# Kernel optimization log

Measured on AMD Instinct MI355X. Metric: run time of the kernel, lower is better.

## Reference

```python
import jax, jax.numpy as jnp
import numpy as np

B, T, X, H, Z, P = 256, 512, 64, 256, 64, 32

_PARAM_SHAPES = [
    ("phi_x_W1", (X, P)), ("phi_x_b1", (P,)), ("phi_x_W2", (P, P)), ("phi_x_b2", (P,)),
    ("phi_z_W", (Z, Z)), ("phi_z_b", (Z,)),
    ("enc_W1", (P + H, H)), ("enc_b1", (H,)), ("enc_W2", (H, H)), ("enc_b2", (H,)),
    ("enc_mean_W", (H, Z)), ("enc_mean_b", (Z,)), ("enc_std_W", (H, Z)), ("enc_std_b", (Z,)),
    ("prior_W", (H, H)), ("prior_b", (H,)),
    ("prior_mean_W", (H, Z)), ("prior_mean_b", (Z,)), ("prior_std_W", (H, Z)), ("prior_std_b", (Z,)),
    ("dec_W1", (Z + H, H)), ("dec_b1", (H,)), ("dec_W2", (H, H)), ("dec_b2", (H,)),
    ("dec_mean_W", (H, X)), ("dec_mean_b", (X,)), ("dec_std_W", (H, X)), ("dec_std_b", (X,)),
    ("gru_K", (P + Z, 3 * H)), ("gru_R", (H, 3 * H)), ("gru_b", (2, 3 * H)),
]


def setup_inputs() -> dict:
    key = jax.random.key(0)
    ks = jax.random.split(key, 4 + len(_PARAM_SHAPES))
    d = {
        "x": jax.random.normal(ks[0], (B, T, X), jnp.float32),
        "y": jax.random.normal(ks[1], (B, T, Z), jnp.float32),
        "domain_labels": jax.random.uniform(ks[2], (B, T, Z), dtype=jnp.float32),
        "eps": jax.random.normal(ks[3], (B, T, Z), jnp.float32),
    }
    for i, (name, shp) in enumerate(_PARAM_SHAPES):
        d[name] = jax.random.normal(ks[4 + i], shp, jnp.float32) * 0.05
    return d


def _vrnn_forward(x, eps,
                  phi_x_W1, phi_x_b1, phi_x_W2, phi_x_b2,
                  phi_z_W, phi_z_b,
                  enc_W1, enc_b1, enc_W2, enc_b2,
                  enc_mean_W, enc_mean_b, enc_std_W, enc_std_b,
                  prior_W, prior_b, prior_mean_W, prior_mean_b, prior_std_W, prior_std_b,
                  dec_W1, dec_b1, dec_W2, dec_b2,
                  dec_mean_W, dec_mean_b, dec_std_W, dec_std_b,
                  gru_K, gru_R, gru_b):
    relu, sp, sig = jax.nn.relu, jax.nn.softplus, jax.nn.sigmoid

    def dense(a, W, b):
        return a @ W + b

    def step(h, inp):
        x_t, eps_t = inp  # [B, X], [B, Z]
        phi_x_t = relu(dense(relu(dense(x_t, phi_x_W1, phi_x_b1)), phi_x_W2, phi_x_b2))
        enc_h = relu(dense(relu(dense(jnp.concatenate([phi_x_t, h], 1), enc_W1, enc_b1)), enc_W2, enc_b2))
        enc_mean_t = dense(enc_h, enc_mean_W, enc_mean_b)
        enc_std_t = sp(dense(enc_h, enc_std_W, enc_std_b))
        pri_h = relu(dense(h, prior_W, prior_b))
        pri_mean_t = dense(pri_h, prior_mean_W, prior_mean_b)
        pri_std_t = sp(dense(pri_h, prior_std_W, prior_std_b))
        z_t = eps_t * enc_std_t + enc_mean_t  # reparameterized sample
        phi_z_t = relu(dense(z_t, phi_z_W, phi_z_b))
        dec_h = relu(dense(relu(dense(jnp.concatenate([phi_z_t, h], 1), dec_W1, dec_b1)), dec_W2, dec_b2))
        dec_mean_t = dense(dec_h, dec_mean_W, dec_mean_b)
        dec_std_t = sp(dense(dec_h, dec_std_W, dec_std_b))
        # Keras GRU cell (reset_after=True): separate input/recurrent biases
        mx = jnp.concatenate([phi_x_t, phi_z_t], 1) @ gru_K + gru_b[0]
        mh = h @ gru_R + gru_b[1]
        xz, xr, xh = jnp.split(mx, 3, axis=1)
        hz, hr, hh = jnp.split(mh, 3, axis=1)
        zg = sig(xz + hz)
        rg = sig(xr + hr)
        h_cand = jnp.tanh(xh + rg * hh)
        h_new = zg * h + (1.0 - zg) * h_cand
        return h_new, (z_t, phi_x_t, enc_mean_t, enc_std_t, dec_mean_t, dec_std_t, pri_mean_t, pri_std_t)

    h0 = jnp.zeros((x.shape[0], gru_R.shape[0]), x.dtype)
    xs = (jnp.swapaxes(x, 0, 1), jnp.swapaxes(eps, 0, 1))  # time-major for scan
    _, outs = jax.lax.scan(step, h0, xs)
    return tuple(jnp.swapaxes(o, 0, 1) for o in outs)  # back to [B, T, .]


def reference(x, y, domain_labels, eps,
              phi_x_W1, phi_x_b1, phi_x_W2, phi_x_b2,
              phi_z_W, phi_z_b,
              enc_W1, enc_b1, enc_W2, enc_b2,
              enc_mean_W, enc_mean_b, enc_std_W, enc_std_b,
              prior_W, prior_b, prior_mean_W, prior_mean_b, prior_std_W, prior_std_b,
              dec_W1, dec_b1, dec_W2, dec_b2,
              dec_mean_W, dec_mean_b, dec_std_W, dec_std_b,
              gru_K, gru_R, gru_b):
    # y and domain_labels are accepted (as in the original __call__) but do not
    # affect the forward math.
    (y_pred, phi_x, enc_mean, enc_std, dec_mean, dec_std, pri_mean, pri_std) = _vrnn_forward(
        x, eps,
        phi_x_W1, phi_x_b1, phi_x_W2, phi_x_b2,
        phi_z_W, phi_z_b,
        enc_W1, enc_b1, enc_W2, enc_b2,
        enc_mean_W, enc_mean_b, enc_std_W, enc_std_b,
        prior_W, prior_b, prior_mean_W, prior_mean_b, prior_std_W, prior_std_b,
        dec_W1, dec_b1, dec_W2, dec_b2,
        dec_mean_W, dec_mean_b, dec_std_W, dec_std_b,
        gru_K, gru_R, gru_b)
    return (y_pred, phi_x, (enc_mean, enc_std), (dec_mean, dec_std), (pri_mean, pri_std))
```

## Files before the change

kernel.cpp:

```cpp
#include <hip/hip_runtime.h>


typedef _Float16 f16;
typedef _Float16 f16x2 __attribute__((ext_vector_type(2)));
typedef _Float16 f16x8 __attribute__((ext_vector_type(8)));
typedef float    f32x4 __attribute__((ext_vector_type(4)));

#define B_  256
#define T_  512
#define BT_ 131072

#define OYP   0u
#define OPHIX 8388608u
#define OENCM 12582912u
#define OENCS 20971520u
#define ODECM 29360128u
#define ODECS 37748736u
#define OPRIM 46137344u
#define OPRIS 54525952u

#define WS_PHIX16 0ull
#define WS_H16    8388608ull
#define WS_PZ16   75497472ull
#define WS_WHB    92274688ull
#define WS_W1TOP  92798976ull
#define WS_KTOP   92815360ull
#define WS_KBOT   92864512ull
#define WS_ENCW2  92962816ull
#define WS_HEADS  93093888ull
#define WS_PHIZW  93159424ull
#define WS_DECW1T 93167616ull
#define WS_DECW2T 93331456ull
#define WS_DECHT  93462528ull
#define WS_PRIWT  93528064ull
#define WS_PRIHT  93659136ull

#if defined(__has_builtin)
#if __has_builtin(__builtin_amdgcn_fdot2)
#define HAVE_FDOT2 1
#endif
#endif

__device__ __forceinline__ float dot8(uint4 w, uint4 h, float acc) {
#ifdef HAVE_FDOT2
    union { uint4 u; f16x2 p[4]; } a, b;
    a.u = w; b.u = h;
    acc = __builtin_amdgcn_fdot2(a.p[0], b.p[0], acc, false);
    acc = __builtin_amdgcn_fdot2(a.p[1], b.p[1], acc, false);
    acc = __builtin_amdgcn_fdot2(a.p[2], b.p[2], acc, false);
    acc = __builtin_amdgcn_fdot2(a.p[3], b.p[3], acc, false);
#else
    union { uint4 u; f16 h8[8]; } a, b;
    a.u = w; b.u = h;
#pragma unroll
    for (int i = 0; i < 8; ++i) acc += (float)a.h8[i] * (float)b.h8[i];
#endif
    return acc;
}

__device__ __forceinline__ float softplus_f(float v) {
    return (v > 15.f) ? v : log1pf(expf(v));
}
__device__ __forceinline__ float sigmoid_f(float v) {
    return 1.f / (1.f + expf(-v));
}

__global__ void pack_loop(const float* __restrict__ src, f16* __restrict__ dst,
                          int K, int Nsrc, int Ndst, int coloff) {
    int idx = blockIdx.x * 256 + threadIdx.x;
    if (idx >= K * Nsrc) return;
    int k = idx / Nsrc, j = idx - k * Nsrc;
    dst[((size_t)(k >> 3) * Ndst + coloff + j) * 8 + (k & 7)] = (f16)src[idx];
}

__global__ void pack_T(const float* __restrict__ src, f16* __restrict__ dst,
                       int K, int N, int noff, int Kd) {
    int idx = blockIdx.x * 256 + threadIdx.x;
    if (idx >= K * N) return;
    int k = idx / N, n = idx - k * N;
    dst[(size_t)(noff + n) * Kd + k] = (f16)src[idx];
}

__global__ void phi_x_kernel(const float* __restrict__ x,
                             const float* __restrict__ W1, const float* __restrict__ b1,
                             const float* __restrict__ W2, const float* __restrict__ b2,
                             float* __restrict__ dout, f16* __restrict__ phix16) {
    size_t row = (size_t)blockIdx.x * 256 + threadIdx.x;
    const float* xr = x + row * 64;
    float l1[32];
#pragma unroll
    for (int j = 0; j < 32; ++j) l1[j] = b1[j];
#pragma unroll 4
    for (int k = 0; k < 64; ++k) {
        float xv = xr[k];
#pragma unroll
        for (int j = 0; j < 32; ++j) l1[j] += xv * W1[k * 32 + j];
    }
#pragma unroll
    for (int j = 0; j < 32; ++j) l1[j] = fmaxf(l1[j], 0.f);
#pragma unroll 4
    for (int j = 0; j < 32; ++j) {
        float acc = b2[j];
#pragma unroll
        for (int k = 0; k < 32; ++k) acc += l1[k] * W2[k * 32 + j];
        acc = fmaxf(acc, 0.f);
        dout[OPHIX + row * 32 + j] = acc;
        phix16[row * 32 + j] = (f16)acc;
    }
}

__launch_bounds__(512)
__global__ void vrnn_recurrent(
    const f16* __restrict__ whb,
    const f16* __restrict__ w1topb,
    const f16* __restrict__ ktopb,
    const f16* __restrict__ kbotb,
    const f16* __restrict__ encw2b,
    const f16* __restrict__ headsb,
    const f16* __restrict__ phizwb,
    const float* __restrict__ enc_b1, const float* __restrict__ enc_b2,
    const float* __restrict__ enc_mean_b, const float* __restrict__ enc_std_b,
    const float* __restrict__ phi_z_b, const float* __restrict__ gru_b,
    const f16* __restrict__ phix16, const float* __restrict__ eps,
    f16* __restrict__ h16, f16* __restrict__ pz16, float* __restrict__ dout) {

    const int tid = threadIdx.x;
    const int r0 = blockIdx.x * 2;

    __shared__ __align__(16) f16 h_sh[2][256];
    __shared__ __align__(16) f16 e1s[2][256];
    __shared__ __align__(16) f16 ehs[2][256];
    __shared__ __align__(16) f16 zps[2][64];
    __shared__ __align__(16) f16 pzs[2][64];
    __shared__ __align__(16) f16 phixs[2][32];
    __shared__ float hf[2][256];
    __shared__ float hs[2][768];
    __shared__ float xsm[2][768];
    __shared__ float ps[1024];
    __shared__ float sb_e1[256], sb_e2[256], sb_hm[128], sb_pz[64];
    __shared__ float sb_bk[768], sb_br[768];

    if (tid < 256) {
        sb_e1[tid] = enc_b1[tid];
        sb_e2[tid] = enc_b2[tid];
        h_sh[0][tid] = (f16)0.f; h_sh[1][tid] = (f16)0.f;
        hf[0][tid] = 0.f; hf[1][tid] = 0.f;
    }
    if (tid < 128) sb_hm[tid] = (tid < 64) ? enc_mean_b[tid] : enc_std_b[tid - 64];
    if (tid < 64)  sb_pz[tid] = phi_z_b[tid];
    { int i = tid; if (i < 768) { sb_bk[i] = gru_b[i]; sb_br[i] = gru_b[768 + i]; } }
    if (tid >= 256) { int i = tid - 256 + 512; if (i < 768) { sb_bk[i] = gru_b[i]; sb_br[i] = gru_b[768 + i]; } }
    if (tid < 32) {
        int r = tid >> 4, d = tid & 15;
        ((unsigned int*)phixs[r])[d] =
            ((const unsigned int*)(phix16 + (size_t)(r0 + r) * T_ * 32))[d];
    }
    float eps_reg = 0.f;
    if (tid < 128) {
        int r = tid >> 6, c = tid & 63;
        eps_reg = eps[((size_t)(r0 + r) * T_) * 64 + c];
    }
    __syncthreads();

    const int mA = (tid >= 256) ? (tid - 256) : -1;
    const int mB = 256 + tid;

    const uint4* whu   = (const uint4*)whb;
    const uint4* w1tu  = (const uint4*)w1topb;
    const uint4* ktu   = (const uint4*)ktopb;
    const uint4* kbu   = (const uint4*)kbotb;
    const uint4* ew2u  = (const uint4*)encw2b;
    const uint4* hdu   = (const uint4*)headsb;
    const uint4* pzwu  = (const uint4*)phizwb;

    for (int t = 0; t < T_; ++t) {
        float a0, a1, b0, b1;
        if (tid < 256) { a0 = sb_e1[tid]; } else { a0 = sb_br[tid - 256]; }
        a1 = a0;
        b0 = sb_br[mB]; b1 = b0;
        const uint4* h0p = (const uint4*)h_sh[0];
        const uint4* h1p = (const uint4*)h_sh[1];
#pragma unroll 4
        for (int kc = 0; kc < 32; ++kc) {
            uint4 hv0 = h0p[kc], hv1 = h1p[kc];
            uint4 wa = whu[kc * 1024 + tid];
            uint4 wb = whu[kc * 1024 + 512 + tid];
            a0 = dot8(wa, hv0, a0); a1 = dot8(wa, hv1, a1);
            b0 = dot8(wb, hv0, b0); b1 = dot8(wb, hv1, b1);
        }
        float xA0 = 0.f, xA1 = 0.f, xB0, xB1;
        xB0 = sb_bk[mB]; xB1 = xB0;
        if (mA >= 0) { xA0 = sb_bk[mA]; xA1 = xA0; }
        const uint4* px0p = (const uint4*)phixs[0];
        const uint4* px1p = (const uint4*)phixs[1];
#pragma unroll
        for (int kc = 0; kc < 4; ++kc) {
            uint4 p0 = px0p[kc], p1 = px1p[kc];
            uint4 wB = ktu[kc * 768 + mB];
            xB0 = dot8(wB, p0, xB0); xB1 = dot8(wB, p1, xB1);
            if (mA >= 0) {
                uint4 wA = ktu[kc * 768 + mA];
                xA0 = dot8(wA, p0, xA0); xA1 = dot8(wA, p1, xA1);
            }
        }
        if (tid < 256) {
#pragma unroll
            for (int kc = 0; kc < 4; ++kc) {
                uint4 p0 = px0p[kc], p1 = px1p[kc];
                uint4 w = w1tu[kc * 256 + tid];
                a0 = dot8(w, p0, a0); a1 = dot8(w, p1, a1);
            }
            e1s[0][tid] = (f16)fmaxf(a0, 0.f);
            e1s[1][tid] = (f16)fmaxf(a1, 0.f);
        } else {
            hs[0][tid - 256] = a0; hs[1][tid - 256] = a1;
        }
        hs[0][mB] = b0; hs[1][mB] = b1;
        __syncthreads();

        {
            int c = tid & 255, kh = tid >> 8;
            float p0 = 0.f, p1 = 0.f;
            const uint4* e0p = (const uint4*)e1s[0];
            const uint4* e1p = (const uint4*)e1s[1];
#pragma unroll 4
            for (int i = 0; i < 16; ++i) {
                int kc = kh * 16 + i;
                uint4 w = ew2u[kc * 256 + c];
                p0 = dot8(w, e0p[kc], p0);
                p1 = dot8(w, e1p[kc], p1);
            }
            ps[(0 * 2 + kh) * 256 + c] = p0;
            ps[(2 + kh) * 256 + c] = p1;
        }
        __syncthreads();
        {
            int r = tid >> 8, j = tid & 255;
            float v = ps[(r * 2) * 256 + j] + ps[(r * 2 + 1) * 256 + j] + sb_e2[j];
            ehs[r][j] = (f16)fmaxf(v, 0.f);
        }
        __syncthreads();

        {
            int c2 = tid & 127, kq = tid >> 7;
            float p0 = 0.f, p1 = 0.f;
            const uint4* h0e = (const uint4*)ehs[0];
            const uint4* h1e = (const uint4*)ehs[1];
#pragma unroll 4
            for (int i = 0; i < 8; ++i) {
                int kc = kq * 8 + i;
                uint4 w = hdu[kc * 128 + c2];
                p0 = dot8(w, h0e[kc], p0);
                p1 = dot8(w, h1e[kc], p1);
            }
            ps[kq * 128 + c2] = p0;
            ps[(4 + kq) * 128 + c2] = p1;
        }
        __syncthreads();
        if (tid < 128) {
            int r = tid >> 6, c = tid & 63;
            float m = sb_hm[c], s = sb_hm[64 + c];
#pragma unroll
            for (int kq = 0; kq < 4; ++kq) {
                m += ps[(r * 4 + kq) * 128 + c];
                s += ps[(r * 4 + kq) * 128 + 64 + c];
            }
            float sp = softplus_f(s);
            float z = eps_reg * sp + m;
            size_t bt = (size_t)(r0 + r) * T_ + t;
            dout[OENCM + bt * 64 + c] = m;
            dout[OENCS + bt * 64 + c] = sp;
            dout[OYP + bt * 64 + c] = z;
            zps[r][c] = (f16)z;
        }
        __syncthreads();

        {
            int c = tid & 63, k8 = tid >> 6;
            uint4 w = pzwu[k8 * 64 + c];
            ps[k8 * 64 + c]       = dot8(w, ((const uint4*)zps[0])[k8], 0.f);
            ps[(8 + k8) * 64 + c] = dot8(w, ((const uint4*)zps[1])[k8], 0.f);
        }
        __syncthreads();
        if (tid < 128) {
            int r = tid >> 6, c = tid & 63;
            float v = sb_pz[c];
#pragma unroll
            for (int k = 0; k < 8; ++k) v += ps[(r * 8 + k) * 64 + c];
            v = fmaxf(v, 0.f);
            pzs[r][c] = (f16)v;
            size_t bt = (size_t)(r0 + r) * T_ + t;
            pz16[bt * 64 + c] = (f16)v;
            if (t + 1 < T_)
                eps_reg = eps[((size_t)(r0 + r) * T_ + (t + 1)) * 64 + c];
        } else if (tid < 160 && (t + 1 < T_)) {
            int r = (tid - 128) >> 4, d = (tid - 128) & 15;
            ((unsigned int*)phixs[r])[d] =
                ((const unsigned int*)(phix16 + ((size_t)(r0 + r) * T_ + (t + 1)) * 32))[d];
        }
        __syncthreads();

        {
            const uint4* p0p = (const uint4*)pzs[0];
            const uint4* p1p = (const uint4*)pzs[1];
#pragma unroll
            for (int kc = 0; kc < 8; ++kc) {
                uint4 p0 = p0p[kc], p1 = p1p[kc];
                uint4 wB = kbu[kc * 768 + mB];
                xB0 = dot8(wB, p0, xB0); xB1 = dot8(wB, p1, xB1);
                if (mA >= 0) {
                    uint4 wA = kbu[kc * 768 + mA];
                    xA0 = dot8(wA, p0, xA0); xA1 = dot8(wA, p1, xA1);
                }
            }
            xsm[0][mB] = xB0; xsm[1][mB] = xB1;
            if (mA >= 0) { xsm[0][mA] = xA0; xsm[1][mA] = xA1; }
        }
        __syncthreads();

        {
            int g = tid & 255, r = tid >> 8;
            float zg = sigmoid_f(xsm[r][g] + hs[r][g]);
            float rg = sigmoid_f(xsm[r][256 + g] + hs[r][256 + g]);
            float hc = tanhf(xsm[r][512 + g] + rg * hs[r][512 + g]);
            float hp = hf[r][g];
            float hn = zg * hp + (1.f - zg) * hc;
            hf[r][g] = hn;
            h_sh[r][g] = (f16)hn;
            size_t bt = (size_t)(r0 + r) * T_ + t;
            h16[bt * 256 + g] = (f16)hp;
        }
        __syncthreads();
    }
}

__launch_bounds__(256)
__global__ void dec_kernel(const f16* __restrict__ h16, const f16* __restrict__ pz16,
                           const f16* __restrict__ w1T, const f16* __restrict__ w2T,
                           const f16* __restrict__ hT,
                           const float* __restrict__ b1, const float* __restrict__ b2,
                           const float* __restrict__ bm, const float* __restrict__ bs,
                           float* __restrict__ dout) {
    __shared__ __align__(16) f16 ht[32][264];
    __shared__ __align__(16) f16 pzt[32][72];
    __shared__ __align__(16) f16 d1[32][264];
    __shared__ __align__(16) f16 d2[32][264];
    const int tid = threadIdx.x;
    const size_t bt0 = (size_t)blockIdx.x * 32;

    {
        int row = tid >> 3, p = tid & 7;
        const uint4* src = (const uint4*)(h16 + (bt0 + row) * 256);
#pragma unroll
        for (int i = 0; i < 4; ++i)
            *(uint4*)&ht[row][(p * 4 + i) * 8] = src[p * 4 + i];
        const uint4* s2 = (const uint4*)(pz16 + (bt0 + row) * 64);
        *(uint4*)&pzt[row][p * 8] = s2[p];
    }
    __syncthreads();

    const int w = tid >> 6, lane = tid & 63;
    const int lm = lane & 15, lk = (lane >> 4) * 8, lr = (lane >> 4) * 4;
    const int n0 = w * 64;

    f32x4 acc[2][4];
#pragma unroll
    for (int ms = 0; ms < 2; ++ms)
#pragma unroll
        for (int ns = 0; ns < 4; ++ns) acc[ms][ns] = (f32x4){0.f, 0.f, 0.f, 0.f};

#pragma unroll
    for (int kc = 0; kc < 2; ++kc) {
        f16x8 A[2];
#pragma unroll
        for (int ms = 0; ms < 2; ++ms) A[ms] = *(const f16x8*)&pzt[ms * 16 + lm][kc * 32 + lk];
#pragma unroll
        for (int ns = 0; ns < 4; ++ns) {
            f16x8 Bf = *(const f16x8*)(w1T + (size_t)(n0 + ns * 16 + lm) * 320 + kc * 32 + lk);
#pragma unroll
            for (int ms = 0; ms < 2; ++ms)
                acc[ms][ns] = __builtin_amdgcn_mfma_f32_16x16x32_f16(A[ms], Bf, acc[ms][ns], 0, 0, 0);
        }
    }
#pragma unroll 2
    for (int kc = 0; kc < 8; ++kc) {
        f16x8 A[2];
#pragma unroll
        for (int ms = 0; ms < 2; ++ms) A[ms] = *(const f16x8*)&ht[ms * 16 + lm][kc * 32 + lk];
#pragma unroll
        for (int ns = 0; ns < 4; ++ns) {
            f16x8 Bf = *(const f16x8*)(w1T + (size_t)(n0 + ns * 16 + lm) * 320 + 64 + kc * 32 + lk);
#pragma unroll
            for (int ms = 0; ms < 2; ++ms)
                acc[ms][ns] = __builtin_amdgcn_mfma_f32_16x16x32_f16(A[ms], Bf, acc[ms][ns], 0, 0, 0);
        }
    }
#pragma unroll
    for (int ns = 0; ns < 4; ++ns) {
        float bv = b1[n0 + ns * 16 + lm];
#pragma unroll
        for (int ms = 0; ms < 2; ++ms)
#pragma unroll
            for (int q = 0; q < 4; ++q)
                d1[ms * 16 + lr + q][n0 + ns * 16 + lm] = (f16)fmaxf(acc[ms][ns][q] + bv, 0.f);
    }
    __syncthreads();

#pragma unroll
    for (int ms = 0; ms < 2; ++ms)
#pragma unroll
        for (int ns = 0; ns < 4; ++ns) acc[ms][ns] = (f32x4){0.f, 0.f, 0.f, 0.f};
#pragma unroll 2
    for (int kc = 0; kc < 8; ++kc) {
        f16x8 A[2];
#pragma unroll
        for (int ms = 0; ms < 2; ++ms) A[ms] = *(const f16x8*)&d1[ms * 16 + lm][kc * 32 + lk];
#pragma unroll
        for (int ns = 0; ns < 4; ++ns) {
            f16x8 Bf = *(const f16x8*)(w2T + (size_t)(n0 + ns * 16 + lm) * 256 + kc * 32 + lk);
#pragma unroll
            for (int ms = 0; ms < 2; ++ms)
                acc[ms][ns] = __builtin_amdgcn_mfma_f32_16x16x32_f16(A[ms], Bf, acc[ms][ns], 0, 0, 0);
        }
    }
#pragma unroll
    for (int ns = 0; ns < 4; ++ns) {
        float bv = b2[n0 + ns * 16 + lm];
#pragma unroll
        for (int ms = 0; ms < 2; ++ms)
#pragma unroll
            for (int q = 0; q < 4; ++q)
                d2[ms * 16 + lr + q][n0 + ns * 16 + lm] = (f16)fmaxf(acc[ms][ns][q] + bv, 0.f);
    }
    __syncthreads();

    if (w < 2) {
        const int n0h = w * 64;
#pragma unroll
        for (int ms = 0; ms < 2; ++ms)
#pragma unroll
            for (int ns = 0; ns < 4; ++ns) acc[ms][ns] = (f32x4){0.f, 0.f, 0.f, 0.f};
#pragma unroll 2
        for (int kc = 0; kc < 8; ++kc) {
            f16x8 A[2];
#pragma unroll
            for (int ms = 0; ms < 2; ++ms) A[ms] = *(const f16x8*)&d2[ms * 16 + lm][kc * 32 + lk];
#pragma unroll
            for (int ns = 0; ns < 4; ++ns) {
                f16x8 Bf = *(const f16x8*)(hT + (size_t)(n0h + ns * 16 + lm) * 256 + kc * 32 + lk);
#pragma unroll
                for (int ms = 0; ms < 2; ++ms)
                    acc[ms][ns] = __builtin_amdgcn_mfma_f32_16x16x32_f16(A[ms], Bf, acc[ms][ns], 0, 0, 0);
            }
        }
#pragma unroll
        for (int ns = 0; ns < 4; ++ns) {
            int n = n0h + ns * 16 + lm;
#pragma unroll
            for (int ms = 0; ms < 2; ++ms)
#pragma unroll
                for (int q = 0; q < 4; ++q) {
                    size_t bt = bt0 + ms * 16 + lr + q;
                    float v = acc[ms][ns][q];
                    if (n < 64) dout[ODECM + bt * 64 + n] = v + bm[n];
                    else        dout[ODECS + bt * 64 + (n - 64)] = softplus_f(v + bs[n - 64]);
                }
        }
    }
}

__launch_bounds__(256)
__global__ void pri_kernel(const f16* __restrict__ h16,
                           const f16* __restrict__ wT, const f16* __restrict__ hT,
                           const float* __restrict__ b1,
                           const float* __restrict__ bm, const float* __restrict__ bs,
                           float* __restrict__ dout) {
    __shared__ __align__(16) f16 ht[32][264];
    __shared__ __align__(16) f16 p1[32][264];
    const int tid = threadIdx.x;
    const size_t bt0 = (size_t)blockIdx.x * 32;
    {
        int row = tid >> 3, p = tid & 7;
        const uint4* src = (const uint4*)(h16 + (bt0 + row) * 256);
#pragma unroll
        for (int i = 0; i < 4; ++i)
            *(uint4*)&ht[row][(p * 4 + i) * 8] = src[p * 4 + i];
    }
    __syncthreads();
    const int w = tid >> 6, lane = tid & 63;
    const int lm = lane & 15, lk = (lane >> 4) * 8, lr = (lane >> 4) * 4;
    const int n0 = w * 64;

    f32x4 acc[2][4];
#pragma unroll
    for (int ms = 0; ms < 2; ++ms)
#pragma unroll
        for (int ns = 0; ns < 4; ++ns) acc[ms][ns] = (f32x4){0.f, 0.f, 0.f, 0.f};
#pragma unroll 2
    for (int kc = 0; kc < 8; ++kc) {
        f16x8 A[2];
#pragma unroll
        for (int ms = 0; ms < 2; ++ms) A[ms] = *(const f16x8*)&ht[ms * 16 + lm][kc * 32 + lk];
#pragma unroll
        for (int ns = 0; ns < 4; ++ns) {
            f16x8 Bf = *(const f16x8*)(wT + (size_t)(n0 + ns * 16 + lm) * 256 + kc * 32 + lk);
#pragma unroll
            for (int ms = 0; ms < 2; ++ms)
                acc[ms][ns] = __builtin_amdgcn_mfma_f32_16x16x32_f16(A[ms], Bf, acc[ms][ns], 0, 0, 0);
        }
    }
#pragma unroll
    for (int ns = 0; ns < 4; ++ns) {
        float bv = b1[n0 + ns * 16 + lm];
#pragma unroll
        for (int ms = 0; ms < 2; ++ms)
#pragma unroll
            for (int q = 0; q < 4; ++q)
                p1[ms * 16 + lr + q][n0 + ns * 16 + lm] = (f16)fmaxf(acc[ms][ns][q] + bv, 0.f);
    }
    __syncthreads();
    if (w < 2) {
        const int n0h = w * 64;
#pragma unroll
        for (int ms = 0; ms < 2; ++ms)
#pragma unroll
            for (int ns = 0; ns < 4; ++ns) acc[ms][ns] = (f32x4){0.f, 0.f, 0.f, 0.f};
#pragma unroll 2
        for (int kc = 0; kc < 8; ++kc) {
            f16x8 A[2];
#pragma unroll
            for (int ms = 0; ms < 2; ++ms) A[ms] = *(const f16x8*)&p1[ms * 16 + lm][kc * 32 + lk];
#pragma unroll
            for (int ns = 0; ns < 4; ++ns) {
                f16x8 Bf = *(const f16x8*)(hT + (size_t)(n0h + ns * 16 + lm) * 256 + kc * 32 + lk);
#pragma unroll
                for (int ms = 0; ms < 2; ++ms)
                    acc[ms][ns] = __builtin_amdgcn_mfma_f32_16x16x32_f16(A[ms], Bf, acc[ms][ns], 0, 0, 0);
            }
        }
#pragma unroll
        for (int ns = 0; ns < 4; ++ns) {
            int n = n0h + ns * 16 + lm;
#pragma unroll
            for (int ms = 0; ms < 2; ++ms)
#pragma unroll
                for (int q = 0; q < 4; ++q) {
                    size_t bt = bt0 + ms * 16 + lr + q;
                    float v = acc[ms][ns][q];
                    if (n < 64) dout[OPRIM + bt * 64 + n] = v + bm[n];
                    else        dout[OPRIS + bt * 64 + (n - 64)] = softplus_f(v + bs[n - 64]);
                }
        }
    }
}

extern "C" void kernel_launch(void* const* d_in, const int* in_sizes, int n_in,
                              void* d_out, int out_size, void* d_ws, size_t ws_size,
                              hipStream_t stream) {
    (void)in_sizes; (void)n_in; (void)out_size; (void)ws_size;
    const float* x          = (const float*)d_in[0];
    const float* eps        = (const float*)d_in[3];
    const float* phi_x_W1   = (const float*)d_in[4];
    const float* phi_x_b1   = (const float*)d_in[5];
    const float* phi_x_W2   = (const float*)d_in[6];
    const float* phi_x_b2   = (const float*)d_in[7];
    const float* phi_z_W    = (const float*)d_in[8];
    const float* phi_z_b    = (const float*)d_in[9];
    const float* enc_W1     = (const float*)d_in[10];
    const float* enc_b1     = (const float*)d_in[11];
    const float* enc_W2     = (const float*)d_in[12];
    const float* enc_b2     = (const float*)d_in[13];
    const float* enc_mean_W = (const float*)d_in[14];
    const float* enc_mean_b = (const float*)d_in[15];
    const float* enc_std_W  = (const float*)d_in[16];
    const float* enc_std_b  = (const float*)d_in[17];
    const float* prior_W    = (const float*)d_in[18];
    const float* prior_b    = (const float*)d_in[19];
    const float* prior_mean_W = (const float*)d_in[20];
    const float* prior_mean_b = (const float*)d_in[21];
    const float* prior_std_W  = (const float*)d_in[22];
    const float* prior_std_b  = (const float*)d_in[23];
    const float* dec_W1     = (const float*)d_in[24];
    const float* dec_b1     = (const float*)d_in[25];
    const float* dec_W2     = (const float*)d_in[26];
    const float* dec_b2     = (const float*)d_in[27];
    const float* dec_mean_W = (const float*)d_in[28];
    const float* dec_mean_b = (const float*)d_in[29];
    const float* dec_std_W  = (const float*)d_in[30];
    const float* dec_std_b  = (const float*)d_in[31];
    const float* gru_K      = (const float*)d_in[32];
    const float* gru_R      = (const float*)d_in[33];
    const float* gru_b      = (const float*)d_in[34];

    float* out = (float*)d_out;
    char* ws = (char*)d_ws;
    f16* phix16 = (f16*)(ws + WS_PHIX16);
    f16* h16    = (f16*)(ws + WS_H16);
    f16* pz16   = (f16*)(ws + WS_PZ16);
    f16* whb    = (f16*)(ws + WS_WHB);
    f16* w1topb = (f16*)(ws + WS_W1TOP);
    f16* ktopb  = (f16*)(ws + WS_KTOP);
    f16* kbotb  = (f16*)(ws + WS_KBOT);
    f16* encw2b = (f16*)(ws + WS_ENCW2);
    f16* headsb = (f16*)(ws + WS_HEADS);
    f16* phizwb = (f16*)(ws + WS_PHIZW);
    f16* decw1T = (f16*)(ws + WS_DECW1T);
    f16* decw2T = (f16*)(ws + WS_DECW2T);
    f16* decht  = (f16*)(ws + WS_DECHT);
    f16* priwT  = (f16*)(ws + WS_PRIWT);
    f16* priht  = (f16*)(ws + WS_PRIHT);

    auto PL = [&](const float* src, f16* dst, int K, int Ns, int Nd, int off) {
        int n = K * Ns;
        pack_loop<<<(n + 255) / 256, 256, 0, stream>>>(src, dst, K, Ns, Nd, off);
    };
    auto PT = [&](const float* src, f16* dst, int K, int N, int noff, int Kd) {
        int n = K * N;
        pack_T<<<(n + 255) / 256, 256, 0, stream>>>(src, dst, K, N, noff, Kd);
    };

    PL(enc_W1 + 32 * 256, whb, 256, 256, 1024, 0);
    PL(gru_R,             whb, 256, 768, 1024, 256);
    PL(enc_W1,   w1topb, 32, 256, 256, 0);
    PL(gru_K,    ktopb,  32, 768, 768, 0);
    PL(gru_K + 32 * 768, kbotb, 64, 768, 768, 0);
    PL(enc_W2,   encw2b, 256, 256, 256, 0);
    PL(enc_mean_W, headsb, 256, 64, 128, 0);
    PL(enc_std_W,  headsb, 256, 64, 128, 64);
    PL(phi_z_W,  phizwb, 64, 64, 64, 0);
    PT(dec_W1, decw1T, 320, 256, 0, 320);
    PT(dec_W2, decw2T, 256, 256, 0, 256);
    PT(dec_mean_W, decht, 256, 64, 0, 256);
    PT(dec_std_W,  decht, 256, 64, 64, 256);
    PT(prior_W, priwT, 256, 256, 0, 256);
    PT(prior_mean_W, priht, 256, 64, 0, 256);
    PT(prior_std_W,  priht, 256, 64, 64, 256);

    phi_x_kernel<<<BT_ / 256, 256, 0, stream>>>(x, phi_x_W1, phi_x_b1, phi_x_W2,
                                                phi_x_b2, out, phix16);

    vrnn_recurrent<<<B_ / 2, 512, 0, stream>>>(
        whb, w1topb, ktopb, kbotb, encw2b, headsb, phizwb,
        enc_b1, enc_b2, enc_mean_b, enc_std_b, phi_z_b, gru_b,
        phix16, eps, h16, pz16, out);

    dec_kernel<<<BT_ / 32, 256, 0, stream>>>(h16, pz16, decw1T, decw2T, decht,
                                             dec_b1, dec_b2, dec_mean_b, dec_std_b, out);
    pri_kernel<<<BT_ / 32, 256, 0, stream>>>(h16, priwT, priht,
                                             prior_b, prior_mean_b, prior_std_b, out);
}
```

Measured before the change: 5.332 ms.

## Stage recurrent weights in LDS/registers, lighten barriers, fuse decoder and prior kernels

In the sequential recurrent kernel, the encoder W2 matrix (128 KB fp16) is copied into shared memory once. Parts of the GRU recurrent weights, the head weights, the phi_z weights and the W1 top slice are kept in registers across all timesteps, so each step no longer re-reads them from global memory. Every __syncthreads is replaced by an inline-asm barrier that waits only on LDS counters, so outstanding global stores are not drained. The decoder and prior kernels are merged into one launch that reuses the loaded h tile. The risks are higher register pressure, possible spills under launch_bounds(512,2), and a 128 KB LDS footprint per block that limits occupancy.

```diff
diff --git a/kernel.cpp b/kernel.cpp
--- a/kernel.cpp
+++ b/kernel.cpp
@@ -9,6 +9,7 @@
 #define B_  256
 #define T_  512
 #define BT_ 131072
+#define NPIN 8
 
 #define OYP   0u
 #define OPHIX 8388608u
@@ -58,6 +59,10 @@
     return acc;
 }
 
+__device__ __forceinline__ void bar_lds() {
+    asm volatile("s_waitcnt lgkmcnt(0)\n\ts_barrier" ::: "memory");
+}
+
 __device__ __forceinline__ float softplus_f(float v) {
     return (v > 15.f) ? v : log1pf(expf(v));
 }
@@ -109,7 +114,7 @@
     }
 }
 
-__launch_bounds__(512)
+__launch_bounds__(512, 2)
 __global__ void vrnn_recurrent(
     const f16* __restrict__ whb,
     const f16* __restrict__ w1topb,
@@ -127,6 +132,7 @@
     const int tid = threadIdx.x;
     const int r0 = blockIdx.x * 2;
 
+    __shared__ __align__(16) f16 encw2s[32 * 256 * 8];
     __shared__ __align__(16) f16 h_sh[2][256];
     __shared__ __align__(16) f16 e1s[2][256];
     __shared__ __align__(16) f16 ehs[2][256];
@@ -140,6 +146,12 @@
     __shared__ float sb_e1[256], sb_e2[256], sb_hm[128], sb_pz[64];
     __shared__ float sb_bk[768], sb_br[768];
 
+    {
+        const uint4* src = (const uint4*)encw2b;
+        uint4* dst = (uint4*)encw2s;
+#pragma unroll
+        for (int i = 0; i < 16; ++i) dst[tid + 512 * i] = src[tid + 512 * i];
+    }
     if (tid < 256) {
         sb_e1[tid] = enc_b1[tid];
         sb_e2[tid] = enc_b2[tid];
@@ -160,18 +172,39 @@
         int r = tid >> 6, c = tid & 63;
         eps_reg = eps[((size_t)(r0 + r) * T_) * 64 + c];
     }
-    __syncthreads();
 
     const int mA = (tid >= 256) ? (tid - 256) : -1;
     const int mB = 256 + tid;
 
-    const uint4* whu   = (const uint4*)whb;
-    const uint4* w1tu  = (const uint4*)w1topb;
-    const uint4* ktu   = (const uint4*)ktopb;
-    const uint4* kbu   = (const uint4*)kbotb;
-    const uint4* ew2u  = (const uint4*)encw2b;
-    const uint4* hdu   = (const uint4*)headsb;
-    const uint4* pzwu  = (const uint4*)phizwb;
+    const uint4* whu  = (const uint4*)whb;
+    const uint4* w1tu = (const uint4*)w1topb;
+    const uint4* ktu  = (const uint4*)ktopb;
+    const uint4* kbu  = (const uint4*)kbotb;
+    const uint4* ew2s = (const uint4*)encw2s;
+    const uint4* hdu  = (const uint4*)headsb;
+    const uint4* pzwu = (const uint4*)phizwb;
+
+    uint4 wpa[NPIN], wpb[NPIN];
+#pragma unroll
+    for (int kc = 0; kc < NPIN; ++kc) {
+        wpa[kc] = whu[kc * 1024 + tid];
+        wpb[kc] = whu[kc * 1024 + 512 + tid];
+    }
+    uint4 hwp[8];
+    {
+        int c2 = tid & 127, kq = tid >> 7;
+#pragma unroll
+        for (int i = 0; i < 8; ++i) hwp[i] = hdu[(kq * 8 + i) * 128 + c2];
+    }
+    uint4 pzwp;
+    { int c = tid & 63, k8 = tid >> 6; pzwp = pzwu[k8 * 64 + c]; }
+    uint4 w1tp[4];
+    if (tid < 256) {
+#pragma unroll
+        for (int i = 0; i < 4; ++i) w1tp[i] = w1tu[i * 256 + tid];
+    }
+
+    __syncthreads();
 
     for (int t = 0; t < T_; ++t) {
         float a0, a1, b0, b1;
@@ -180,8 +213,14 @@
         b0 = sb_br[mB]; b1 = b0;
         const uint4* h0p = (const uint4*)h_sh[0];
         const uint4* h1p = (const uint4*)h_sh[1];
+#pragma unroll
+        for (int kc = 0; kc < NPIN; ++kc) {
+            uint4 hv0 = h0p[kc], hv1 = h1p[kc];
+            a0 = dot8(wpa[kc], hv0, a0); a1 = dot8(wpa[kc], hv1, a1);
+            b0 = dot8(wpb[kc], hv0, b0); b1 = dot8(wpb[kc], hv1, b1);
+        }
 #pragma unroll 4
-        for (int kc = 0; kc < 32; ++kc) {
+        for (int kc = NPIN; kc < 32; ++kc) {
             uint4 hv0 = h0p[kc], hv1 = h1p[kc];
             uint4 wa = whu[kc * 1024 + tid];
             uint4 wb = whu[kc * 1024 + 512 + tid];
@@ -207,8 +246,7 @@
 #pragma unroll
             for (int kc = 0; kc < 4; ++kc) {
                 uint4 p0 = px0p[kc], p1 = px1p[kc];
-                uint4 w = w1tu[kc * 256 + tid];
-                a0 = dot8(w, p0, a0); a1 = dot8(w, p1, a1);
+                a0 = dot8(w1tp[kc], p0, a0); a1 = dot8(w1tp[kc], p1, a1);
             }
             e1s[0][tid] = (f16)fmaxf(a0, 0.f);
             e1s[1][tid] = (f16)fmaxf(a1, 0.f);
@@ -216,7 +254,7 @@
             hs[0][tid - 256] = a0; hs[1][tid - 256] = a1;
         }
         hs[0][mB] = b0; hs[1][mB] = b1;
-        __syncthreads();
+        bar_lds();
 
         {
             int c = tid & 255, kh = tid >> 8;
@@ -226,37 +264,36 @@
 #pragma unroll 4
             for (int i = 0; i < 16; ++i) {
                 int kc = kh * 16 + i;
-                uint4 w = ew2u[kc * 256 + c];
+                uint4 w = ew2s[kc * 256 + c];
                 p0 = dot8(w, e0p[kc], p0);
                 p1 = dot8(w, e1p[kc], p1);
             }
-            ps[(0 * 2 + kh) * 256 + c] = p0;
+            ps[kh * 256 + c] = p0;
             ps[(2 + kh) * 256 + c] = p1;
         }
-        __syncthreads();
+        bar_lds();
         {
             int r = tid >> 8, j = tid & 255;
             float v = ps[(r * 2) * 256 + j] + ps[(r * 2 + 1) * 256 + j] + sb_e2[j];
             ehs[r][j] = (f16)fmaxf(v, 0.f);
         }
-        __syncthreads();
+        bar_lds();
 
         {
             int c2 = tid & 127, kq = tid >> 7;
             float p0 = 0.f, p1 = 0.f;
             const uint4* h0e = (const uint4*)ehs[0];
             const uint4* h1e = (const uint4*)ehs[1];
-#pragma unroll 4
+#pragma unroll
             for (int i = 0; i < 8; ++i) {
                 int kc = kq * 8 + i;
-                uint4 w = hdu[kc * 128 + c2];
-                p0 = dot8(w, h0e[kc], p0);
-                p1 = dot8(w, h1e[kc], p1);
+                p0 = dot8(hwp[i], h0e[kc], p0);
+                p1 = dot8(hwp[i], h1e[kc], p1);
             }
             ps[kq * 128 + c2] = p0;
             ps[(4 + kq) * 128 + c2] = p1;
         }
-        __syncthreads();
+        bar_lds();
         if (tid < 128) {
             int r = tid >> 6, c = tid & 63;
             float m = sb_hm[c], s = sb_hm[64 + c];
@@ -273,15 +310,14 @@
             dout[OYP + bt * 64 + c] = z;
             zps[r][c] = (f16)z;
         }
-        __syncthreads();
+        bar_lds();
 
         {
             int c = tid & 63, k8 = tid >> 6;
-            uint4 w = pzwu[k8 * 64 + c];
-            ps[k8 * 64 + c]       = dot8(w, ((const uint4*)zps[0])[k8], 0.f);
-            ps[(8 + k8) * 64 + c] = dot8(w, ((const uint4*)zps[1])[k8], 0.f);
-        }
-        __syncthreads();
+            ps[k8 * 64 + c]       = dot8(pzwp, ((const uint4*)zps[0])[k8], 0.f);
+            ps[(8 + k8) * 64 + c] = dot8(pzwp, ((const uint4*)zps[1])[k8], 0.f);
+        }
+        bar_lds();
         if (tid < 128) {
             int r = tid >> 6, c = tid & 63;
             float v = sb_pz[c];
@@ -298,7 +334,7 @@
             ((unsigned int*)phixs[r])[d] =
                 ((const unsigned int*)(phix16 + ((size_t)(r0 + r) * T_ + (t + 1)) * 32))[d];
         }
-        __syncthreads();
+        bar_lds();
 
         {
             const uint4* p0p = (const uint4*)pzs[0];
@@ -316,7 +352,7 @@
             xsm[0][mB] = xB0; xsm[1][mB] = xB1;
             if (mA >= 0) { xsm[0][mA] = xA0; xsm[1][mA] = xA1; }
         }
-        __syncthreads();
+        bar_lds();
 
         {
             int g = tid & 255, r = tid >> 8;
@@ -330,17 +366,20 @@
             size_t bt = (size_t)(r0 + r) * T_ + t;
             h16[bt * 256 + g] = (f16)hp;
         }
-        __syncthreads();
+        bar_lds();
     }
 }
 
 __launch_bounds__(256)
-__global__ void dec_kernel(const f16* __restrict__ h16, const f16* __restrict__ pz16,
-                           const f16* __restrict__ w1T, const f16* __restrict__ w2T,
-                           const f16* __restrict__ hT,
-                           const float* __restrict__ b1, const float* __restrict__ b2,
-                           const float* __restrict__ bm, const float* __restrict__ bs,
-                           float* __restrict__ dout) {
+__global__ void decpri_kernel(const f16* __restrict__ h16, const f16* __restrict__ pz16,
+                              const f16* __restrict__ w1T, const f16* __restrict__ w2T,
+                              const f16* __restrict__ dhT,
+                              const f16* __restrict__ priwT, const f16* __restrict__ prihT,
+                              const float* __restrict__ db1, const float* __restrict__ db2,
+                              const float* __restrict__ dbm, const float* __restrict__ dbs,
+                              const float* __restrict__ pb1,
+                              const float* __restrict__ pbm, const float* __restrict__ pbs,
+                              float* __restrict__ dout) {
     __shared__ __align__(16) f16 ht[32][264];
     __shared__ __align__(16) f16 pzt[32][72];
     __shared__ __align__(16) f16 d1[32][264];
@@ -364,11 +403,11 @@
     const int n0 = w * 64;
 
     f32x4 acc[2][4];
+
 #pragma unroll
     for (int ms = 0; ms < 2; ++ms)
 #pragma unroll
         for (int ns = 0; ns < 4; ++ns) acc[ms][ns] = (f32x4){0.f, 0.f, 0.f, 0.f};
-
 #pragma unroll
     for (int kc = 0; kc < 2; ++kc) {
         f16x8 A[2];
@@ -397,7 +436,7 @@
     }
 #pragma unroll
     for (int ns = 0; ns < 4; ++ns) {
-        float bv = b1[n0 + ns * 16 + lm];
+        float bv = db1[n0 + ns * 16 + lm];
 #pragma unroll
         for (int ms = 0; ms < 2; ++ms)
 #pragma unroll
@@ -425,7 +464,7 @@
     }
 #pragma unroll
     for (int ns = 0; ns < 4; ++ns) {
-        float bv = b2[n0 + ns * 16 + lm];
+        float bv = db2[n0 + ns * 16 + lm];
 #pragma unroll
         for (int ms = 0; ms < 2; ++ms)
 #pragma unroll
@@ -447,7 +486,7 @@
             for (int ms = 0; ms < 2; ++ms) A[ms] = *(const f16x8*)&d2[ms * 16 + lm][kc * 32 + lk];
 #pragma unroll
             for (int ns = 0; ns < 4; ++ns) {
-                f16x8 Bf = *(const f16x8*)(hT + (size_t)(n0h + ns * 16 + lm) * 256 + kc * 32 + lk);
+                f16x8 Bf = *(const f16x8*)(dhT + (size_t)(n0h + ns * 16 + lm) * 256 + kc * 32 + lk);
 #pragma unroll
                 for (int ms = 0; ms < 2; ++ms)
                     acc[ms][ns] = __builtin_amdgcn_mfma_f32_16x16x32_f16(A[ms], Bf, acc[ms][ns], 0, 0, 0);
@@ -462,36 +501,11 @@
                 for (int q = 0; q < 4; ++q) {
                     size_t bt = bt0 + ms * 16 + lr + q;
                     float v = acc[ms][ns][q];
-                    if (n < 64) dout[ODECM + bt * 64 + n] = v + bm[n];
-                    else        dout[ODECS + bt * 64 + (n - 64)] = softplus_f(v + bs[n - 64]);
+                    if (n < 64) dout[ODECM + bt * 64 + n] = v + dbm[n];
+                    else        dout[ODECS + bt * 64 + (n - 64)] = softplus_f(v + dbs[n - 64]);
                 }
         }
     }
-}
-
-__launch_bounds__(256)
-__global__ void pri_kernel(const f16* __restrict__ h16,
-                           const f16* __restrict__ wT, const f16* __restrict__ hT,
-                           const float* __restrict__ b1,
-                           const float* __restrict__ bm, const float* __restrict__ bs,
-                           float* __restrict__ dout) {
-    __shared__ __align__(16) f16 ht[32][264];
-    __shared__ __align__(16) f16 p1[32][264];
-    const int tid = threadIdx.x;
-    const size_t bt0 = (size_t)blockIdx.x * 32;
-    {
-        int row = tid >> 3, p = tid & 7;
-        const uint4* src = (const uint4*)(h16 + (bt0 + row) * 256);
-#pragma unroll
-        for (int i = 0; i < 4; ++i)
-            *(uint4*)&ht[row][(p * 4 + i) * 8] = src[p * 4 + i];
-    }
-    __syncthreads();
-    const int w = tid >> 6, lane = tid & 63;
-    const int lm = lane & 15, lk = (lane >> 4) * 8, lr = (lane >> 4) * 4;
-    const int n0 = w * 64;
-
-    f32x4 acc[2][4];
 #pragma unroll
     for (int ms = 0; ms < 2; ++ms)
 #pragma unroll
@@ -503,7 +517,7 @@
         for (int ms = 0; ms < 2; ++ms) A[ms] = *(const f16x8*)&ht[ms * 16 + lm][kc * 32 + lk];
 #pragma unroll
         for (int ns = 0; ns < 4; ++ns) {
-            f16x8 Bf = *(const f16x8*)(wT + (size_t)(n0 + ns * 16 + lm) * 256 + kc * 32 + lk);
+            f16x8 Bf = *(const f16x8*)(priwT + (size_t)(n0 + ns * 16 + lm) * 256 + kc * 32 + lk);
 #pragma unroll
             for (int ms = 0; ms < 2; ++ms)
                 acc[ms][ns] = __builtin_amdgcn_mfma_f32_16x16x32_f16(A[ms], Bf, acc[ms][ns], 0, 0, 0);
@@ -511,14 +525,15 @@
     }
 #pragma unroll
     for (int ns = 0; ns < 4; ++ns) {
-        float bv = b1[n0 + ns * 16 + lm];
+        float bv = pb1[n0 + ns * 16 + lm];
 #pragma unroll
         for (int ms = 0; ms < 2; ++ms)
 #pragma unroll
             for (int q = 0; q < 4; ++q)
-                p1[ms * 16 + lr + q][n0 + ns * 16 + lm] = (f16)fmaxf(acc[ms][ns][q] + bv, 0.f);
+                d1[ms * 16 + lr + q][n0 + ns * 16 + lm] = (f16)fmaxf(acc[ms][ns][q] + bv, 0.f);
     }
     __syncthreads();
+
     if (w < 2) {
         const int n0h = w * 64;
 #pragma unroll
@@ -529,10 +544,10 @@
         for (int kc = 0; kc < 8; ++kc) {
             f16x8 A[2];
 #pragma unroll
-            for (int ms = 0; ms < 2; ++ms) A[ms] = *(const f16x8*)&p1[ms * 16 + lm][kc * 32 + lk];
+            for (int ms = 0; ms < 2; ++ms) A[ms] = *(const f16x8*)&d1[ms * 16 + lm][kc * 32 + lk];
 #pragma unroll
             for (int ns = 0; ns < 4; ++ns) {
-                f16x8 Bf = *(const f16x8*)(hT + (size_t)(n0h + ns * 16 + lm) * 256 + kc * 32 + lk);
+                f16x8 Bf = *(const f16x8*)(prihT + (size_t)(n0h + ns * 16 + lm) * 256 + kc * 32 + lk);
 #pragma unroll
                 for (int ms = 0; ms < 2; ++ms)
                     acc[ms][ns] = __builtin_amdgcn_mfma_f32_16x16x32_f16(A[ms], Bf, acc[ms][ns], 0, 0, 0);
@@ -547,8 +562,8 @@
                 for (int q = 0; q < 4; ++q) {
                     size_t bt = bt0 + ms * 16 + lr + q;
                     float v = acc[ms][ns][q];
-                    if (n < 64) dout[OPRIM + bt * 64 + n] = v + bm[n];
-                    else        dout[OPRIS + bt * 64 + (n - 64)] = softplus_f(v + bs[n - 64]);
+                    if (n < 64) dout[OPRIM + bt * 64 + n] = v + pbm[n];
+                    else        dout[OPRIS + bt * 64 + (n - 64)] = softplus_f(v + pbs[n - 64]);
                 }
         }
     }
@@ -644,8 +659,8 @@
         enc_b1, enc_b2, enc_mean_b, enc_std_b, phi_z_b, gru_b,
         phix16, eps, h16, pz16, out);
 
-    dec_kernel<<<BT_ / 32, 256, 0, stream>>>(h16, pz16, decw1T, decw2T, decht,
-                                             dec_b1, dec_b2, dec_mean_b, dec_std_b, out);
-    pri_kernel<<<BT_ / 32, 256, 0, stream>>>(h16, priwT, priht,
-                                             prior_b, prior_mean_b, prior_std_b, out);
-}
+    decpri_kernel<<<BT_ / 32, 256, 0, stream>>>(h16, pz16, decw1T, decw2T, decht,
+                                                priwT, priht,
+                                                dec_b1, dec_b2, dec_mean_b, dec_std_b,
+                                                prior_b, prior_mean_b, prior_std_b, out);
+}
```

Result: slower. 8.730 ms (+63.7%).
